# Performance work log

Measured on AMD Instinct MI355X. Metric: run time of the kernel, lower is better.

The kernel has to match this reference:

```python
import jax, jax.numpy as jnp
import numpy as np

T, E, IN, OUT, A, R = 16384, 8, 1024, 1024, 8, 16  # tokens, experts, d_in, d_out, adapters, lora rank


def prepare_routing(x, indices, num_groups):
    """Sort tokens by group index; return sorted x, per-group counts, unsort map, sorted ids."""
    sort_idx = jnp.argsort(indices)  # stable sort keeps within-group order
    x_sorted = x[sort_idx]
    group_sizes = jnp.bincount(indices, length=num_groups).astype(jnp.int32)
    unsort_indices = jnp.argsort(sort_idx)
    return x_sorted, group_sizes, unsort_indices, indices[sort_idx]


def setup_inputs() -> dict:
    key = jax.random.key(0)
    ks = jax.random.split(key, 6)
    # tokens pre-sorted by expert: group_sizes must sum to T exactly
    expert_ids = jnp.sort(jax.random.randint(ks[0], (T,), 0, E))
    group_sizes = jnp.bincount(expert_ids, length=E).astype(jnp.int32)
    x = jax.random.normal(ks[1], (T, IN), jnp.float32)
    adapter_indices_sorted = jax.random.randint(ks[2], (T,), 0, A)
    weight = jax.random.normal(ks[3], (E, IN, OUT), jnp.float32) * 0.02
    lora_A = jax.random.normal(ks[4], (A, E, IN, R), jnp.float32) * 0.02
    lora_B = jax.random.normal(ks[5], (A, E, R, OUT), jnp.float32) * 0.02
    lora_scaling = jnp.ones((A,), jnp.float32)
    return {
        "x": x,
        "group_sizes": group_sizes,
        "adapter_indices_sorted": adapter_indices_sorted,
        "weight": weight,
        "lora_A": lora_A,
        "lora_B": lora_B,
        "lora_scaling": lora_scaling,
    }


def reference(x, group_sizes, adapter_indices_sorted, weight, lora_A, lora_B, lora_scaling):
    # base grouped GEMM over experts: [T,IN] x [E,IN,OUT] -> [T,OUT]
    base_out = jax.lax.ragged_dot(x, weight, group_sizes)

    # per-token expert id from contiguous group sizes
    expert_ids = jnp.repeat(jnp.arange(E), group_sizes, total_repeat_length=T)
    flattened = expert_ids * A + adapter_indices_sorted  # expert-major (E,A) group id

    # flatten adapters x experts into E*A groups (expert-major to match flattened ids)
    A_mat = lora_A.transpose(1, 0, 2, 3).reshape(E * A, IN, R)
    B_mat = lora_B.transpose(1, 0, 2, 3).reshape(E * A, R, OUT)

    x_sorted, combined_gs, unsort_indices, _ = prepare_routing(x, flattened, E * A)
    inter = jax.lax.ragged_dot(x_sorted, A_mat, combined_gs)          # [T,R]
    lora_out_sorted = jax.lax.ragged_dot(inter, B_mat, combined_gs)   # [T,OUT]
    lora_out = lora_out_sorted[unsort_indices]
    lora_out = lora_out * lora_scaling[adapter_indices_sorted][:, None]
    return base_out + lora_out
```

## Files before the change

### kernel.cpp

```cpp
#include <hip/hip_runtime.h>

#define T_TOK 16384
#define NEXP 8
#define DIN 1024
#define DOUT 1024
#define NADP 8
#define RANK 16
#define NGRP 64
#define NP1 520
#define BK 64
#define NKSTEP 16

typedef float f32x4 __attribute__((ext_vector_type(4)));
typedef float f32x16 __attribute__((ext_vector_type(16)));
typedef __bf16 bf16x8 __attribute__((ext_vector_type(8)));

typedef __attribute__((address_space(3))) void lds_void;
typedef __attribute__((address_space(1))) void g_void;

static __device__ __forceinline__ unsigned short f2bf(float f) {
    union { float f; unsigned u; } c; c.f = f;
    unsigned r = c.u + 0x7FFFu + ((c.u >> 16) & 1u);
    return (unsigned short)(r >> 16);
}

__global__ __launch_bounds__(256) void k_prep(const float* __restrict__ lA,
                                              unsigned short* __restrict__ Agt) {
    __shared__ __attribute__((aligned(16))) unsigned short lds_u[16 * 1032];
    int g = blockIdx.x;
    int t = threadIdx.x;
    int a = g & 7, e = g >> 3;
    const float* src = lA + (size_t)(a * NEXP + e) * DIN * RANK;
#pragma unroll
    for (int it = 0; it < 4; it++) {
        int k = it * 256 + t;
        const float4* p = (const float4*)(src + (size_t)k * RANK);
        float4 v0 = p[0], v1 = p[1], v2 = p[2], v3 = p[3];
        lds_u[0 * 1032 + k] = f2bf(v0.x);  lds_u[1 * 1032 + k] = f2bf(v0.y);
        lds_u[2 * 1032 + k] = f2bf(v0.z);  lds_u[3 * 1032 + k] = f2bf(v0.w);
        lds_u[4 * 1032 + k] = f2bf(v1.x);  lds_u[5 * 1032 + k] = f2bf(v1.y);
        lds_u[6 * 1032 + k] = f2bf(v1.z);  lds_u[7 * 1032 + k] = f2bf(v1.w);
        lds_u[8 * 1032 + k] = f2bf(v2.x);  lds_u[9 * 1032 + k] = f2bf(v2.y);
        lds_u[10 * 1032 + k] = f2bf(v2.z); lds_u[11 * 1032 + k] = f2bf(v2.w);
        lds_u[12 * 1032 + k] = f2bf(v3.x); lds_u[13 * 1032 + k] = f2bf(v3.y);
        lds_u[14 * 1032 + k] = f2bf(v3.z); lds_u[15 * 1032 + k] = f2bf(v3.w);
    }
    __syncthreads();
    unsigned short* dst = Agt + (size_t)g * RANK * DIN;
    int r = t >> 4, ks = (t & 15) * 64;
#pragma unroll
    for (int j = 0; j < 8; j++)
        *(uint4*)(dst + r * DIN + ks + j * 8) = *(const uint4*)&lds_u[r * 1032 + ks + j * 8];
}

#define XB2 2048
#define NBW 2048
__global__ __launch_bounds__(256) void k_mega(const float* __restrict__ x,
                                              const float* __restrict__ W,
                                              const float* __restrict__ lB,
                                              const unsigned short* __restrict__ Agt,
                                              const int* __restrict__ gs,
                                              const int* __restrict__ aidx,
                                              const float* __restrict__ scal,
                                              unsigned short* __restrict__ xb,
                                              unsigned short* __restrict__ Wt,
                                              unsigned short* __restrict__ Blt,
                                              unsigned short* __restrict__ interb) {
    __shared__ __attribute__((aligned(16))) unsigned short lds_u[16 * 1032];
    int b = blockIdx.x;
    int t = threadIdx.x;
    if (b < NP1) {
        int e = -1, m0 = 0, valid = 0;
        {
            int acc_t = 0, base = 0;
#pragma unroll
            for (int ee = 0; ee < NEXP; ee++) {
                int sz = gs[ee];
                int nt = (sz + 31) >> 5;
                if (e < 0 && b < acc_t + nt) {
                    int loc = b - acc_t;
                    e = ee; m0 = base + (loc << 5);
                    int v = sz - (loc << 5); valid = v > 32 ? 32 : v;
                }
                acc_t += nt; base += sz;
            }
        }
        if (e < 0) return;

        int lane = t & 63, w = t >> 6;
        int ln = lane & 15, q = lane >> 4;

        const unsigned short* A0 = Agt + ((size_t)(e * NADP + 2 * w) * RANK + ln) * DIN + q * 8;
        const unsigned short* A1 = A0 + (size_t)RANK * DIN;
        int r0 = m0 + ln;       if (r0 >= T_TOK) r0 = T_TOK - 1;
        int r1 = m0 + 16 + ln;  if (r1 >= T_TOK) r1 = T_TOK - 1;
        const float* X0 = x + (size_t)r0 * DIN + q * 8;
        const float* X1 = x + (size_t)r1 * DIN + q * 8;

        f32x4 acc[2][2];
#pragma unroll
        for (int i = 0; i < 2; i++) {
            acc[i][0] = (f32x4){0.f, 0.f, 0.f, 0.f};
            acc[i][1] = (f32x4){0.f, 0.f, 0.f, 0.f};
        }

#pragma unroll 4
        for (int k0 = 0; k0 < DIN; k0 += 32) {
            bf16x8 b0 = *(const bf16x8*)(A0 + k0);
            bf16x8 b1 = *(const bf16x8*)(A1 + k0);
#pragma unroll
            for (int rg = 0; rg < 2; rg++) {
                const float* xp = (rg == 0) ? (X0 + k0) : (X1 + k0);
                float4 u0 = *(const float4*)xp;
                float4 u1 = *(const float4*)(xp + 4);
                unsigned short af_u[8];
                af_u[0] = f2bf(u0.x); af_u[1] = f2bf(u0.y); af_u[2] = f2bf(u0.z); af_u[3] = f2bf(u0.w);
                af_u[4] = f2bf(u1.x); af_u[5] = f2bf(u1.y); af_u[6] = f2bf(u1.z); af_u[7] = f2bf(u1.w);
                bf16x8 af = *(const bf16x8*)af_u;
                acc[rg][0] = __builtin_amdgcn_mfma_f32_16x16x32_bf16(b0, af, acc[rg][0], 0, 0, 0);
                acc[rg][1] = __builtin_amdgcn_mfma_f32_16x16x32_bf16(b1, af, acc[rg][1], 0, 0, 0);
            }
        }

        float s0 = scal[2 * w], s1 = scal[2 * w + 1];
#pragma unroll
        for (int rg = 0; rg < 2; rg++) {
            int tr = rg * 16 + ln;
            if (tr < valid) {
                int tok = m0 + tr;
                int a = aidx[tok];
                if (a == 2 * w) {
                    f32x4 v = acc[rg][0];
                    ushort4 u;
                    u.x = f2bf(s0 * v[0]); u.y = f2bf(s0 * v[1]);
                    u.z = f2bf(s0 * v[2]); u.w = f2bf(s0 * v[3]);
                    *(ushort4*)(interb + (size_t)tok * RANK + q * 4) = u;
                } else if (a == 2 * w + 1) {
                    f32x4 v = acc[rg][1];
                    ushort4 u;
                    u.x = f2bf(s1 * v[0]); u.y = f2bf(s1 * v[1]);
                    u.z = f2bf(s1 * v[2]); u.w = f2bf(s1 * v[3]);
                    *(ushort4*)(interb + (size_t)tok * RANK + q * 4) = u;
                }
            }
        }
    } else if (b < NP1 + XB2) {
        int bx = b - NP1;
        const size_t total = (size_t)(T_TOK + 128) * DIN / 4;
        const size_t conv  = (size_t)T_TOK * DIN / 4;
        size_t gid = (size_t)bx * 256 + t;
#pragma unroll
        for (int it = 0; it < 9; it++) {
            size_t u = gid + (size_t)it * (XB2 * 256);
            if (u < total) {
                ushort4 o;
                if (u < conv) {
                    float4 v = *(const float4*)(x + u * 4);
                    o.x = f2bf(v.x); o.y = f2bf(v.y); o.z = f2bf(v.z); o.w = f2bf(v.w);
                } else {
                    o.x = 0; o.y = 0; o.z = 0; o.w = 0;
                }
                *(ushort4*)(xb + u * 4) = o;
            }
        }
    } else if (b < NP1 + XB2 + NBW) {
        int idx = b - (NP1 + XB2);
        int e = idx >> 8;
        int k0 = ((idx >> 4) & 15) * 64, n0 = (idx & 15) * 64;
        const float* We = W + (size_t)e * DIN * DOUT;
        unsigned short* Wte = Wt + (size_t)e * DIN * DOUT;
        unsigned* lds32 = (unsigned*)lds_u;
        int kp = t >> 3;
        int nc = (t & 7) * 8;
        const float* r0 = We + (size_t)(k0 + 2 * kp) * DOUT + n0 + nc;
        const float* r1 = r0 + DOUT;
        float4 a0 = *(const float4*)r0, a1 = *(const float4*)(r0 + 4);
        float4 c0 = *(const float4*)r1, c1 = *(const float4*)(r1 + 4);
        lds32[(nc + 0) * 34 + kp] = (unsigned)f2bf(a0.x) | ((unsigned)f2bf(c0.x) << 16);
        lds32[(nc + 1) * 34 + kp] = (unsigned)f2bf(a0.y) | ((unsigned)f2bf(c0.y) << 16);
        lds32[(nc + 2) * 34 + kp] = (unsigned)f2bf(a0.z) | ((unsigned)f2bf(c0.z) << 16);
        lds32[(nc + 3) * 34 + kp] = (unsigned)f2bf(a0.w) | ((unsigned)f2bf(c0.w) << 16);
        lds32[(nc + 4) * 34 + kp] = (unsigned)f2bf(a1.x) | ((unsigned)f2bf(c1.x) << 16);
        lds32[(nc + 5) * 34 + kp] = (unsigned)f2bf(a1.y) | ((unsigned)f2bf(c1.y) << 16);
        lds32[(nc + 6) * 34 + kp] = (unsigned)f2bf(a1.z) | ((unsigned)f2bf(c1.z) << 16);
        lds32[(nc + 7) * 34 + kp] = (unsigned)f2bf(a1.w) | ((unsigned)f2bf(c1.w) << 16);
        __syncthreads();
        int n = t >> 2, kq = (t & 3) * 8;
        uint2 d0 = *(const uint2*)&lds32[n * 34 + kq + 0];
        uint2 d1 = *(const uint2*)&lds32[n * 34 + kq + 2];
        uint2 d2 = *(const uint2*)&lds32[n * 34 + kq + 4];
        uint2 d3 = *(const uint2*)&lds32[n * 34 + kq + 6];
        uint4 v0; v0.x = d0.x; v0.y = d0.y; v0.z = d1.x; v0.w = d1.y;
        uint4 v1; v1.x = d2.x; v1.y = d2.y; v1.z = d3.x; v1.w = d3.y;
        *(uint4*)(Wte + (size_t)(n0 + n) * DIN + k0 + kq * 2) = v0;
        *(uint4*)(Wte + (size_t)(n0 + n) * DIN + k0 + kq * 2 + 8) = v1;
    } else {
        int idx = b - (NP1 + XB2 + NBW);
        int e = idx >> 3, nc = idx & 7;
        int k = t >> 1, half = t & 1;
        int a = k >> 4, r = k & 15;
        const float* src = lB + ((size_t)(a * NEXP + e) * RANK + r) * DOUT + nc * 128 + half * 64;
#pragma unroll
        for (int j = 0; j < 16; j++) {
            float4 v = *(const float4*)(src + j * 4);
            int nl = half * 64 + j * 4;
            lds_u[k * 129 + nl + 0] = f2bf(v.x);
            lds_u[k * 129 + nl + 1] = f2bf(v.y);
            lds_u[k * 129 + nl + 2] = f2bf(v.z);
            lds_u[k * 129 + nl + 3] = f2bf(v.w);
        }
        __syncthreads();
        int nl = t >> 1, kh = t & 1;
        unsigned short* dst = Blt + ((size_t)(e * 1024 + nc * 128 + nl)) * 128 + kh * 64;
#pragma unroll
        for (int g2 = 0; g2 < 8; g2++) {
            uint4 pv;
            unsigned short s0 = lds_u[(kh * 64 + g2 * 8 + 0) * 129 + nl];
            unsigned short s1 = lds_u[(kh * 64 + g2 * 8 + 1) * 129 + nl];
            unsigned short s2 = lds_u[(kh * 64 + g2 * 8 + 2) * 129 + nl];
            unsigned short s3 = lds_u[(kh * 64 + g2 * 8 + 3) * 129 + nl];
            unsigned short s4 = lds_u[(kh * 64 + g2 * 8 + 4) * 129 + nl];
            unsigned short s5 = lds_u[(kh * 64 + g2 * 8 + 5) * 129 + nl];
            unsigned short s6 = lds_u[(kh * 64 + g2 * 8 + 6) * 129 + nl];
            unsigned short s7 = lds_u[(kh * 64 + g2 * 8 + 7) * 129 + nl];
            pv.x = (unsigned)s0 | ((unsigned)s1 << 16);
            pv.y = (unsigned)s2 | ((unsigned)s3 << 16);
            pv.z = (unsigned)s4 | ((unsigned)s5 << 16);
            pv.w = (unsigned)s6 | ((unsigned)s7 << 16);
            *(uint4*)(dst + g2 * 8) = pv;
        }
    }
}

__global__ __launch_bounds__(256) void k_gemm(const unsigned short* __restrict__ xb,
                                              const unsigned short* __restrict__ wt,
                                              const int* __restrict__ gs,
                                              const unsigned short* __restrict__ interb,
                                              const int* __restrict__ aidx,
                                              const unsigned short* __restrict__ Blt,
                                              float* __restrict__ out) {
    __shared__ __attribute__((aligned(16))) unsigned short smem[32768];

    int id = blockIdx.y * 8 + blockIdx.x;
    int xcd = id & 7;
    int j = id >> 3;
    int tileid = xcd * 17 + (j >> 3);
    int n0 = (j & 7) * 128;

    int e = -1, m0 = 0, valid = 0;
    {
        int acc_t = 0, base = 0;
#pragma unroll
        for (int ee = 0; ee < NEXP; ee++) {
            int sz = gs[ee];
            int nt = (sz + 127) >> 7;
            if (e < 0 && tileid < acc_t + nt) {
                int loc = tileid - acc_t;
                e = ee; m0 = base + (loc << 7);
                int v = sz - (loc << 7); valid = v > 128 ? 128 : v;
            }
            acc_t += nt; base += sz;
        }
    }
    if (e < 0) return;

    int t = threadIdx.x;
    int lane = t & 63;
    int wave = t >> 6;
    int wm = wave >> 1, wn = wave & 1;
    int r32 = lane & 31, hi = lane >> 5;

    const unsigned short* wte = wt + (size_t)e * DIN * DOUT;

    f32x16 acc[2][2];
#pragma unroll
    for (int i = 0; i < 2; i++)
#pragma unroll
        for (int j2 = 0; j2 < 2; j2++) acc[i][j2] = (f32x16)(0.f);

    int srow = wave * 16 + (lane >> 2);
    int skoff = (((lane & 3) ^ ((lane >> 2) ^ (lane >> 4))) & 3) * 8;
    const unsigned short* gA = xb + (size_t)m0 * DIN;
    const unsigned short* gB = wte + (size_t)n0 * DIN;

    auto STAGE = [&](int buf, int k0) {
#pragma unroll
        for (int jj = 0; jj < 2; jj++) {
            int row = jj * 64 + srow;
            __builtin_amdgcn_global_load_lds(
                (const g_void*)(gA + (size_t)row * DIN + k0 + skoff),
                (lds_void*)((char*)smem + buf * 16384 + jj * 4096 + wave * 1024), 16, 0, 0);
            __builtin_amdgcn_global_load_lds(
                (const g_void*)(gB + (size_t)row * DIN + k0 + skoff),
                (lds_void*)((char*)smem + buf * 16384 + 8192 + jj * 4096 + wave * 1024), 16, 0, 0);
        }
    };

    int fr = (r32 ^ (r32 >> 2)) & 3;

    auto COMPUTE16 = [&](int buf) {
        const char* Ab = (const char*)smem + buf * 16384;
        const char* Bb = Ab + 8192;
#pragma unroll
        for (int kf = 0; kf < 2; kf++) {
            int kc = kf * 2 + hi;
            int slot = (kc ^ fr) * 16;
            bf16x8 af[2], bfr[2];
#pragma unroll
            for (int mi = 0; mi < 2; mi++) {
                int row = wm * 64 + mi * 32 + r32;
                af[mi] = *(const bf16x8*)(Ab + row * 64 + slot);
            }
#pragma unroll
            for (int ni = 0; ni < 2; ni++) {
                int row = wn * 64 + ni * 32 + r32;
                bfr[ni] = *(const bf16x8*)(Bb + row * 64 + slot);
            }
#pragma unroll
            for (int mi = 0; mi < 2; mi++)
#pragma unroll
                for (int ni = 0; ni < 2; ni++)
                    acc[mi][ni] = __builtin_amdgcn_mfma_f32_32x32x16_bf16(af[mi], bfr[ni], acc[mi][ni], 0, 0, 0);
        }
    };

    STAGE(0, 0);  STAGE(1, 32);
    STAGE(2, 64); STAGE(3, 96);
#pragma unroll
    for (int ts = 0; ts < NKSTEP; ts++) {
        if (ts < NKSTEP - 1) asm volatile("s_waitcnt vmcnt(8)" ::: "memory");
        else                 asm volatile("s_waitcnt vmcnt(0)" ::: "memory");
        __builtin_amdgcn_s_barrier();
        int p = ts & 1;
        __builtin_amdgcn_s_setprio(1);
        COMPUTE16(2 * p);
        COMPUTE16(2 * p + 1);
        __builtin_amdgcn_s_setprio(0);
        if (ts < NKSTEP - 2) {
            __builtin_amdgcn_s_barrier();
            STAGE(2 * p,     (ts + 2) * BK);
            STAGE(2 * p + 1, (ts + 2) * BK + 32);
        }
    }

    {
        int row = t >> 1, h = t & 1;
        int rs = row & 15;
        uint4 z = {0u, 0u, 0u, 0u};
        uint4 payload = z;
        int pslot = -1;
        if (row < valid) {
            int tok = m0 + row;
            int a = aidx[tok];
            payload = *(const uint4*)(interb + (size_t)tok * RANK + h * 8);
            pslot = a * 2 + h;
        }
#pragma unroll
        for (int l2 = 0; l2 < 8; l2++) {
            int l = l2 * 2 + h;
            int phys = l ^ rs;
            *(uint4*)((char*)smem + row * 256 + phys * 16) = (l == pslot) ? payload : z;
        }
    }
    __syncthreads();
#pragma unroll
    for (int kf = 0; kf < 8; kf++) {
        int kc = kf * 2 + hi;
        bf16x8 af[2], bfr[2];
#pragma unroll
        for (int ni = 0; ni < 2; ni++) {
            int n = wn * 64 + ni * 32 + r32;
            bfr[ni] = *(const bf16x8*)(Blt + ((size_t)(e * 1024 + n0 + n)) * 128 + kc * 8);
        }
#pragma unroll
        for (int mi = 0; mi < 2; mi++) {
            int row = wm * 64 + mi * 32 + r32;
            int slot = kc ^ (r32 & 15);
            af[mi] = *(const bf16x8*)((const char*)smem + row * 256 + slot * 16);
        }
#pragma unroll
        for (int mi = 0; mi < 2; mi++)
#pragma unroll
            for (int ni = 0; ni < 2; ni++)
                acc[mi][ni] = __builtin_amdgcn_mfma_f32_32x32x16_bf16(af[mi], bfr[ni], acc[mi][ni], 0, 0, 0);
    }

#pragma unroll
    for (int mi = 0; mi < 2; mi++) {
#pragma unroll
        for (int r = 0; r < 16; r++) {
            int row32 = (r & 3) + 8 * (r >> 2) + 4 * hi;
            int row_l = wm * 64 + mi * 32 + row32;
            if (row_l < valid) {
                float* orow = out + (size_t)(m0 + row_l) * DOUT + n0 + wn * 64 + r32;
#pragma unroll
                for (int ni = 0; ni < 2; ni++)
                    orow[ni * 32] = acc[mi][ni][r];
            }
        }
    }
}

extern "C" void kernel_launch(void* const* d_in, const int* in_sizes, int n_in,
                              void* d_out, int out_size, void* d_ws, size_t ws_size,
                              hipStream_t stream) {
    (void)in_sizes; (void)n_in; (void)out_size; (void)ws_size;
    const float* x    = (const float*)d_in[0];
    const int*   gs   = (const int*)d_in[1];
    const int*   aidx = (const int*)d_in[2];
    const float* W    = (const float*)d_in[3];
    const float* lA   = (const float*)d_in[4];
    const float* lB   = (const float*)d_in[5];
    const float* scal = (const float*)d_in[6];
    float* out = (float*)d_out;

    char* ws = (char*)d_ws;
    unsigned short* xb     = (unsigned short*)ws;        size_t o = 33816576;
    unsigned short* wt     = (unsigned short*)(ws + o);  o += 16777216;
    unsigned short* Agt    = (unsigned short*)(ws + o);  o += 2097152;
    unsigned short* Blt    = (unsigned short*)(ws + o);  o += 2097152;
    unsigned short* interb = (unsigned short*)(ws + o);  o += 524288;

    k_prep<<<NGRP, 256, 0, stream>>>(lA, Agt);
    k_mega<<<NP1 + XB2 + NBW + 64, 256, 0, stream>>>(x, W, lB, Agt, gs, aidx, scal,
                                                     xb, wt, Blt, interb);
    k_gemm<<<dim3(8, 136), 256, 0, stream>>>(xb, wt, gs, interb, aidx, Blt, out);
}
```

Baseline: 266.4 us.

## Fuse x bf16 conversion into LoRA-A pass and move B prep to k_prep

```diff
diff --git a/kernel.cpp b/kernel.cpp
--- a/kernel.cpp
+++ b/kernel.cpp
@@ -25,48 +25,85 @@
 }
 
 __global__ __launch_bounds__(256) void k_prep(const float* __restrict__ lA,
-                                              unsigned short* __restrict__ Agt) {
+                                              const float* __restrict__ lB,
+                                              unsigned short* __restrict__ Agt,
+                                              unsigned short* __restrict__ Blt) {
     __shared__ __attribute__((aligned(16))) unsigned short lds_u[16 * 1032];
-    int g = blockIdx.x;
+    int b = blockIdx.x;
     int t = threadIdx.x;
-    int a = g & 7, e = g >> 3;
-    const float* src = lA + (size_t)(a * NEXP + e) * DIN * RANK;
-#pragma unroll
-    for (int it = 0; it < 4; it++) {
-        int k = it * 256 + t;
-        const float4* p = (const float4*)(src + (size_t)k * RANK);
-        float4 v0 = p[0], v1 = p[1], v2 = p[2], v3 = p[3];
-        lds_u[0 * 1032 + k] = f2bf(v0.x);  lds_u[1 * 1032 + k] = f2bf(v0.y);
-        lds_u[2 * 1032 + k] = f2bf(v0.z);  lds_u[3 * 1032 + k] = f2bf(v0.w);
-        lds_u[4 * 1032 + k] = f2bf(v1.x);  lds_u[5 * 1032 + k] = f2bf(v1.y);
-        lds_u[6 * 1032 + k] = f2bf(v1.z);  lds_u[7 * 1032 + k] = f2bf(v1.w);
-        lds_u[8 * 1032 + k] = f2bf(v2.x);  lds_u[9 * 1032 + k] = f2bf(v2.y);
-        lds_u[10 * 1032 + k] = f2bf(v2.z); lds_u[11 * 1032 + k] = f2bf(v2.w);
-        lds_u[12 * 1032 + k] = f2bf(v3.x); lds_u[13 * 1032 + k] = f2bf(v3.y);
-        lds_u[14 * 1032 + k] = f2bf(v3.z); lds_u[15 * 1032 + k] = f2bf(v3.w);
-    }
-    __syncthreads();
-    unsigned short* dst = Agt + (size_t)g * RANK * DIN;
-    int r = t >> 4, ks = (t & 15) * 64;
-#pragma unroll
-    for (int j = 0; j < 8; j++)
-        *(uint4*)(dst + r * DIN + ks + j * 8) = *(const uint4*)&lds_u[r * 1032 + ks + j * 8];
+    if (b < NGRP) {
+        int g = b;
+        int a = g & 7, e = g >> 3;
+        const float* src = lA + (size_t)(a * NEXP + e) * DIN * RANK;
+#pragma unroll
+        for (int it = 0; it < 4; it++) {
+            int k = it * 256 + t;
+            const float4* p = (const float4*)(src + (size_t)k * RANK);
+            float4 v0 = p[0], v1 = p[1], v2 = p[2], v3 = p[3];
+            lds_u[0 * 1032 + k] = f2bf(v0.x);  lds_u[1 * 1032 + k] = f2bf(v0.y);
+            lds_u[2 * 1032 + k] = f2bf(v0.z);  lds_u[3 * 1032 + k] = f2bf(v0.w);
+            lds_u[4 * 1032 + k] = f2bf(v1.x);  lds_u[5 * 1032 + k] = f2bf(v1.y);
+            lds_u[6 * 1032 + k] = f2bf(v1.z);  lds_u[7 * 1032 + k] = f2bf(v1.w);
+            lds_u[8 * 1032 + k] = f2bf(v2.x);  lds_u[9 * 1032 + k] = f2bf(v2.y);
+            lds_u[10 * 1032 + k] = f2bf(v2.z); lds_u[11 * 1032 + k] = f2bf(v2.w);
+            lds_u[12 * 1032 + k] = f2bf(v3.x); lds_u[13 * 1032 + k] = f2bf(v3.y);
+            lds_u[14 * 1032 + k] = f2bf(v3.z); lds_u[15 * 1032 + k] = f2bf(v3.w);
+        }
+        __syncthreads();
+        unsigned short* dst = Agt + (size_t)g * RANK * DIN;
+        int r = t >> 4, ks = (t & 15) * 64;
+#pragma unroll
+        for (int j = 0; j < 8; j++)
+            *(uint4*)(dst + r * DIN + ks + j * 8) = *(const uint4*)&lds_u[r * 1032 + ks + j * 8];
+    } else {
+        int idx = b - NGRP;
+        int e = idx >> 3, nc = idx & 7;
+        int k = t >> 1, half = t & 1;
+        int a = k >> 4, r = k & 15;
+        const float* src = lB + ((size_t)(a * NEXP + e) * RANK + r) * DOUT + nc * 128 + half * 64;
+#pragma unroll
+        for (int j = 0; j < 16; j++) {
+            float4 v = *(const float4*)(src + j * 4);
+            int nl = half * 64 + j * 4;
+            lds_u[k * 129 + nl + 0] = f2bf(v.x);
+            lds_u[k * 129 + nl + 1] = f2bf(v.y);
+            lds_u[k * 129 + nl + 2] = f2bf(v.z);
+            lds_u[k * 129 + nl + 3] = f2bf(v.w);
+        }
+        __syncthreads();
+        int nl = t >> 1, kh = t & 1;
+        unsigned short* dst = Blt + ((size_t)(e * 1024 + nc * 128 + nl)) * 128 + kh * 64;
+#pragma unroll
+        for (int g2 = 0; g2 < 8; g2++) {
+            uint4 pv;
+            unsigned short s0 = lds_u[(kh * 64 + g2 * 8 + 0) * 129 + nl];
+            unsigned short s1 = lds_u[(kh * 64 + g2 * 8 + 1) * 129 + nl];
+            unsigned short s2 = lds_u[(kh * 64 + g2 * 8 + 2) * 129 + nl];
+            unsigned short s3 = lds_u[(kh * 64 + g2 * 8 + 3) * 129 + nl];
+            unsigned short s4 = lds_u[(kh * 64 + g2 * 8 + 4) * 129 + nl];
+            unsigned short s5 = lds_u[(kh * 64 + g2 * 8 + 5) * 129 + nl];
+            unsigned short s6 = lds_u[(kh * 64 + g2 * 8 + 6) * 129 + nl];
+            unsigned short s7 = lds_u[(kh * 64 + g2 * 8 + 7) * 129 + nl];
+            pv.x = (unsigned)s0 | ((unsigned)s1 << 16);
+            pv.y = (unsigned)s2 | ((unsigned)s3 << 16);
+            pv.z = (unsigned)s4 | ((unsigned)s5 << 16);
+            pv.w = (unsigned)s6 | ((unsigned)s7 << 16);
+            *(uint4*)(dst + g2 * 8) = pv;
+        }
+    }
 }
 
-#define XB2 2048
 #define NBW 2048
 __global__ __launch_bounds__(256) void k_mega(const float* __restrict__ x,
                                               const float* __restrict__ W,
-                                              const float* __restrict__ lB,
                                               const unsigned short* __restrict__ Agt,
                                               const int* __restrict__ gs,
                                               const int* __restrict__ aidx,
                                               const float* __restrict__ scal,
                                               unsigned short* __restrict__ xb,
                                               unsigned short* __restrict__ Wt,
-                                              unsigned short* __restrict__ Blt,
                                               unsigned short* __restrict__ interb) {
-    __shared__ __attribute__((aligned(16))) unsigned short lds_u[16 * 1032];
+    __shared__ __attribute__((aligned(16))) unsigned lds32[64 * 34];
     int b = blockIdx.x;
     int t = threadIdx.x;
     if (b < NP1) {
@@ -92,10 +129,14 @@
 
         const unsigned short* A0 = Agt + ((size_t)(e * NADP + 2 * w) * RANK + ln) * DIN + q * 8;
         const unsigned short* A1 = A0 + (size_t)RANK * DIN;
-        int r0 = m0 + ln;       if (r0 >= T_TOK) r0 = T_TOK - 1;
-        int r1 = m0 + 16 + ln;  if (r1 >= T_TOK) r1 = T_TOK - 1;
+        int row0 = m0 + ln;
+        int row1 = m0 + 16 + ln;
+        int r0 = row0 >= T_TOK ? T_TOK - 1 : row0;
+        int r1 = row1 >= T_TOK ? T_TOK - 1 : row1;
         const float* X0 = x + (size_t)r0 * DIN + q * 8;
         const float* X1 = x + (size_t)r1 * DIN + q * 8;
+        unsigned short* xb0 = xb + (size_t)row0 * DIN + q * 8;
+        unsigned short* xb1 = xb + (size_t)row1 * DIN + q * 8;
 
         f32x4 acc[2][2];
 #pragma unroll
@@ -117,6 +158,11 @@
                 af_u[0] = f2bf(u0.x); af_u[1] = f2bf(u0.y); af_u[2] = f2bf(u0.z); af_u[3] = f2bf(u0.w);
                 af_u[4] = f2bf(u1.x); af_u[5] = f2bf(u1.y); af_u[6] = f2bf(u1.z); af_u[7] = f2bf(u1.w);
                 bf16x8 af = *(const bf16x8*)af_u;
+                if (w == 0) {
+                    int rowa = (rg == 0) ? row0 : row1;
+                    if (rowa < T_TOK)
+                        *(bf16x8*)(((rg == 0) ? xb0 : xb1) + k0) = af;
+                }
                 acc[rg][0] = __builtin_amdgcn_mfma_f32_16x16x32_bf16(b0, af, acc[rg][0], 0, 0, 0);
                 acc[rg][1] = __builtin_amdgcn_mfma_f32_16x16x32_bf16(b1, af, acc[rg][1], 0, 0, 0);
             }
@@ -144,32 +190,12 @@
                 }
             }
         }
-    } else if (b < NP1 + XB2) {
-        int bx = b - NP1;
-        const size_t total = (size_t)(T_TOK + 128) * DIN / 4;
-        const size_t conv  = (size_t)T_TOK * DIN / 4;
-        size_t gid = (size_t)bx * 256 + t;
-#pragma unroll
-        for (int it = 0; it < 9; it++) {
-            size_t u = gid + (size_t)it * (XB2 * 256);
-            if (u < total) {
-                ushort4 o;
-                if (u < conv) {
-                    float4 v = *(const float4*)(x + u * 4);
-                    o.x = f2bf(v.x); o.y = f2bf(v.y); o.z = f2bf(v.z); o.w = f2bf(v.w);
-                } else {
-                    o.x = 0; o.y = 0; o.z = 0; o.w = 0;
-                }
-                *(ushort4*)(xb + u * 4) = o;
-            }
-        }
-    } else if (b < NP1 + XB2 + NBW) {
-        int idx = b - (NP1 + XB2);
+    } else if (b < NP1 + NBW) {
+        int idx = b - NP1;
         int e = idx >> 8;
         int k0 = ((idx >> 4) & 15) * 64, n0 = (idx & 15) * 64;
         const float* We = W + (size_t)e * DIN * DOUT;
         unsigned short* Wte = Wt + (size_t)e * DIN * DOUT;
-        unsigned* lds32 = (unsigned*)lds_u;
         int kp = t >> 3;
         int nc = (t & 7) * 8;
         const float* r0 = We + (size_t)(k0 + 2 * kp) * DOUT + n0 + nc;
@@ -195,40 +221,12 @@
         *(uint4*)(Wte + (size_t)(n0 + n) * DIN + k0 + kq * 2) = v0;
         *(uint4*)(Wte + (size_t)(n0 + n) * DIN + k0 + kq * 2 + 8) = v1;
     } else {
-        int idx = b - (NP1 + XB2 + NBW);
-        int e = idx >> 3, nc = idx & 7;
-        int k = t >> 1, half = t & 1;
-        int a = k >> 4, r = k & 15;
-        const float* src = lB + ((size_t)(a * NEXP + e) * RANK + r) * DOUT + nc * 128 + half * 64;
-#pragma unroll
-        for (int j = 0; j < 16; j++) {
-            float4 v = *(const float4*)(src + j * 4);
-            int nl = half * 64 + j * 4;
-            lds_u[k * 129 + nl + 0] = f2bf(v.x);
-            lds_u[k * 129 + nl + 1] = f2bf(v.y);
-            lds_u[k * 129 + nl + 2] = f2bf(v.z);
-            lds_u[k * 129 + nl + 3] = f2bf(v.w);
-        }
-        __syncthreads();
-        int nl = t >> 1, kh = t & 1;
-        unsigned short* dst = Blt + ((size_t)(e * 1024 + nc * 128 + nl)) * 128 + kh * 64;
-#pragma unroll
-        for (int g2 = 0; g2 < 8; g2++) {
-            uint4 pv;
-            unsigned short s0 = lds_u[(kh * 64 + g2 * 8 + 0) * 129 + nl];
-            unsigned short s1 = lds_u[(kh * 64 + g2 * 8 + 1) * 129 + nl];
-            unsigned short s2 = lds_u[(kh * 64 + g2 * 8 + 2) * 129 + nl];
-            unsigned short s3 = lds_u[(kh * 64 + g2 * 8 + 3) * 129 + nl];
-            unsigned short s4 = lds_u[(kh * 64 + g2 * 8 + 4) * 129 + nl];
-            unsigned short s5 = lds_u[(kh * 64 + g2 * 8 + 5) * 129 + nl];
-            unsigned short s6 = lds_u[(kh * 64 + g2 * 8 + 6) * 129 + nl];
-            unsigned short s7 = lds_u[(kh * 64 + g2 * 8 + 7) * 129 + nl];
-            pv.x = (unsigned)s0 | ((unsigned)s1 << 16);
-            pv.y = (unsigned)s2 | ((unsigned)s3 << 16);
-            pv.z = (unsigned)s4 | ((unsigned)s5 << 16);
-            pv.w = (unsigned)s6 | ((unsigned)s7 << 16);
-            *(uint4*)(dst + g2 * 8) = pv;
-        }
+        int idx = b - (NP1 + NBW);
+        ushort4* base = (ushort4*)(xb + (size_t)T_TOK * DIN);
+        ushort4 z = {0, 0, 0, 0};
+#pragma unroll
+        for (int it = 0; it < 4; it++)
+            base[(size_t)idx * 1024 + it * 256 + t] = z;
     }
 }
 
@@ -421,8 +419,7 @@
     unsigned short* Blt    = (unsigned short*)(ws + o);  o += 2097152;
     unsigned short* interb = (unsigned short*)(ws + o);  o += 524288;
 
-    k_prep<<<NGRP, 256, 0, stream>>>(lA, Agt);
-    k_mega<<<NP1 + XB2 + NBW + 64, 256, 0, stream>>>(x, W, lB, Agt, gs, aidx, scal,
-                                                     xb, wt, Blt, interb);
+    k_prep<<<NGRP + 64, 256, 0, stream>>>(lA, lB, Agt, Blt);
+    k_mega<<<NP1 + NBW + 32, 256, 0, stream>>>(x, W, Agt, gs, aidx, scal, xb, wt, interb);
     k_gemm<<<dim3(8, 136), 256, 0, stream>>>(xb, wt, gs, interb, aidx, Blt, out);
 }
```

Result: slower. 280.0 us (+5.1%).
